# Kernel optimization log

Measured on AMD Instinct MI355X. Metric: run time of the kernel, lower is better.

Reference implementation:

```python
import jax, jax.numpy as jnp
from jax import lax
import numpy as np

B, T, I, H = 256, 512, 512, 1024

def setup_inputs() -> dict:
    key = jax.random.key(0)
    ks = jax.random.split(key, 6)
    s_ih = 1.0 / np.sqrt(H)
    return {
        "x": jax.random.normal(ks[0], (B, T, I), dtype=jnp.float32),
        "W_ih": jax.random.uniform(ks[1], (4 * H, I), minval=-s_ih, maxval=s_ih, dtype=jnp.float32),
        "W_hh": jax.random.uniform(ks[2], (4 * H, H), minval=-s_ih, maxval=s_ih, dtype=jnp.float32),
        "b_ih": jax.random.uniform(ks[3], (4 * H,), minval=-s_ih, maxval=s_ih, dtype=jnp.float32),
        "b_hh": jax.random.uniform(ks[4], (4 * H,), minval=-s_ih, maxval=s_ih, dtype=jnp.float32),
        "c0": jax.random.normal(ks[5], (B, H), dtype=jnp.float32),  # torch code inits cell state with randn
    }

def reference(x, W_ih, W_hh, b_ih, b_hh, c0):
    # Faithful to LSTMBody.forward: h0 = zeros, c0 = randn (provided as input),
    # per-step nn.LSTMCell; returns the final CELL state (the torch code's `out`).
    h0 = jnp.zeros((x.shape[0], W_hh.shape[1]), dtype=x.dtype)
    Wi_T = W_ih.T  # [I, 4H]
    Wh_T = W_hh.T  # [H, 4H]
    b = b_ih + b_hh

    def step(carry, xt):
        h, c = carry
        gates = xt @ Wi_T + h @ Wh_T + b  # [B, 4H]
        i, f, g, o = jnp.split(gates, 4, axis=-1)  # PyTorch gate order: i, f, g, o
        c_new = jax.nn.sigmoid(f) * c + jax.nn.sigmoid(i) * jnp.tanh(g)
        h_new = jax.nn.sigmoid(o) * jnp.tanh(c_new)
        return (h_new, c_new), None

    xs = jnp.swapaxes(x, 0, 1)  # [T, B, I] for scan over time
    (h, c), _ = lax.scan(step, (h0, c0), xs)
    return c
```

## Files before the change

kernel.cpp:

```cpp
#include <hip/hip_runtime.h>
#include <stdint.h>

#define Bsz 256
#define Tsz 512
#define Isz 512
#define Hsz 1024

typedef __attribute__((ext_vector_type(8))) short short8;
typedef __attribute__((ext_vector_type(4))) float f32x4;

static constexpr size_t XBF_OFF  = 0;
static constexpr size_t WIBF_OFF = 134217728;
static constexpr size_t HBUF_OFF = 138412032;
static constexpr size_t FLAG_OFF = 139460608;
static constexpr size_t WS_NEED  = 139493376;

__device__ __forceinline__ unsigned short f2bf(float f) {
  union { float f; unsigned u; } v; v.f = f;
  unsigned r = v.u + 0x7fff + ((v.u >> 16) & 1);
  return (unsigned short)(r >> 16);
}

__device__ __forceinline__ void cvt8(const float* __restrict__ s, unsigned short* __restrict__ d) {
  float4 a = *(const float4*)s;
  float4 b = *(const float4*)(s + 4);
  union { unsigned short us[8]; uint4 v; } o;
  o.us[0] = f2bf(a.x); o.us[1] = f2bf(a.y); o.us[2] = f2bf(a.z); o.us[3] = f2bf(a.w);
  o.us[4] = f2bf(b.x); o.us[5] = f2bf(b.y); o.us[6] = f2bf(b.z); o.us[7] = f2bf(b.w);
  *(uint4*)d = o.v;
}

__device__ __forceinline__ short8 ld_h(const unsigned short* p) {
  unsigned long long lo = __hip_atomic_load((unsigned long long*)(void*)p,
                                            __ATOMIC_RELAXED, __HIP_MEMORY_SCOPE_AGENT);
  unsigned long long hi = __hip_atomic_load((unsigned long long*)(void*)(p + 4),
                                            __ATOMIC_RELAXED, __HIP_MEMORY_SCOPE_AGENT);
  union { unsigned long long q[2]; short8 s; } u;
  u.q[0] = lo; u.q[1] = hi;
  return u.s;
}

__device__ __forceinline__ unsigned ld_flag(const unsigned* p) {
  return __hip_atomic_load((unsigned*)p, __ATOMIC_RELAXED, __HIP_MEMORY_SCOPE_AGENT);
}

__global__ __launch_bounds__(256)
void init_kernel(const float* __restrict__ x, const float* __restrict__ Wi,
                 unsigned char* __restrict__ ws)
{
  unsigned short* xbf  = (unsigned short*)(ws + XBF_OFF);
  unsigned short* wibf = (unsigned short*)(ws + WIBF_OFF);
  const int bid = blockIdx.x;
  const int tid = threadIdx.x;

  if (bid < 32768) {
    const int rowid = bid * 4 + (tid >> 6);
    const int t = rowid >> 8;
    const int b = rowid & 255;
    const int i = (tid & 63) * 8;
    const float* src = x + ((size_t)b * Tsz + t) * Isz + i;
    unsigned short* dst = xbf + (size_t)rowid * Isz + i;
    cvt8(src, dst);
  } else if (bid < 32768 + 1024) {
    const size_t base = (size_t)(bid - 32768) * 2048 + (size_t)tid * 8;
    cvt8(Wi + base, wibf + base);
  } else {
    const int z = bid - 33792;
    uint4 zero = make_uint4(0u, 0u, 0u, 0u);
    for (size_t j = (size_t)z * 256 + tid; j < 67584; j += (size_t)260 * 256)
      ((uint4*)(ws + HBUF_OFF))[j] = zero;
  }
}

__global__ __launch_bounds__(512, 2)
void lstm_persistent(const float* __restrict__ Wh,
                     const float* __restrict__ b_ih, const float* __restrict__ b_hh,
                     const float* __restrict__ c0, float* __restrict__ out,
                     unsigned char* __restrict__ ws)
{
  const unsigned short* __restrict__ xbf  = (const unsigned short*)(ws + XBF_OFF);
  const unsigned short* __restrict__ wibf = (const unsigned short*)(ws + WIBF_OFF);
  unsigned short* __restrict__ hbuf = (unsigned short*)(ws + HBUF_OFF);
  unsigned* __restrict__ flags = (unsigned*)(ws + FLAG_OFF);

  __shared__ unsigned short WhT[64][1032];
  __shared__ float red[4][64][17];
  __shared__ float bias[64];

  const int tid  = threadIdx.x;
  const int bid  = blockIdx.x;
  const int cg   = bid & 63;
  const int rg   = bid >> 6;
  const int wv    = tid >> 6;
  const int wv4   = wv & 3;
  const int khalf = wv >> 2;
  const int lane = tid & 63;
  const int l16  = lane & 15;
  const int quad = lane >> 4;

  {
    const int n  = tid >> 3;
    const int q  = n >> 4, u = n & 15;
    const int gc = q * 1024 + cg * 16 + u;
    const int k0 = (tid & 7) * 128;
    const float* src = Wh + (size_t)gc * Hsz + k0;
    unsigned short* dst = &WhT[n][k0];
    #pragma unroll 4
    for (int k = 0; k < 128; k += 8) cvt8(src + k, dst + k);
  }
  if (tid < 64) {
    const int q = tid >> 4, u = tid & 15;
    const int gc = q * 1024 + cg * 16 + u;
    bias[tid] = b_ih[gc] + b_hh[gc];
  }
  __syncthreads();

  const int rowbase = rg * 64 + wv4 * 16;
  const int arow    = rowbase + l16;
  const int hcol    = cg * 16 + l16;

  unsigned* const flag_base = flags + (size_t)rg * 2048 + (size_t)wv4 * 8;
  unsigned* const myslot    = flag_base + (size_t)cg * 32;
  unsigned* const pollp     = flag_base + (size_t)(khalf * 32 + (lane & 31)) * 32;

  const float bi_r = bias[l16];
  const float bf_r = bias[16 + l16];
  const float bg_r = bias[32 + l16];
  const float bo_r = bias[48 + l16];

  float creg[4] = {0.f, 0.f, 0.f, 0.f};
  if (khalf == 0) {
    #pragma unroll
    for (int r = 0; r < 4; ++r)
      creg[r] = c0[(size_t)(rowbase + quad * 4 + r) * Hsz + hcol];
  }

  const unsigned short* bp[4];
  #pragma unroll
  for (int q = 0; q < 4; ++q)
    bp[q] = wibf + (size_t)(q * 1024 + cg * 16 + l16) * Isz + khalf * 256 + quad * 8;

  int p = 0;
  for (int t = 0; t < Tsz; ++t) {
    const unsigned short* xt = xbf  + (size_t)t * Bsz * Isz + (size_t)arow * Isz
                                    + khalf * 256 + quad * 8;
    const unsigned short* hp = hbuf + (size_t)p * Bsz * Hsz + (size_t)arow * Hsz
                                    + khalf * 512 + quad * 8;
    const unsigned tgt = (unsigned)t;

    f32x4 acc[4];
    #pragma unroll
    for (int q = 0; q < 4; ++q) acc[q] = (f32x4){0.f, 0.f, 0.f, 0.f};

    #pragma unroll
    for (int ks = 0; ks < 8; ++ks) {
      const int kk = ks * 32;
      short8 av = *(const short8*)(xt + kk);
      short8 b0 = *(const short8*)(bp[0] + kk);
      short8 b1 = *(const short8*)(bp[1] + kk);
      short8 b2 = *(const short8*)(bp[2] + kk);
      short8 b3 = *(const short8*)(bp[3] + kk);
      acc[0] = __builtin_amdgcn_mfma_f32_16x16x32_bf16(av, b0, acc[0], 0, 0, 0);
      acc[1] = __builtin_amdgcn_mfma_f32_16x16x32_bf16(av, b1, acc[1], 0, 0, 0);
      acc[2] = __builtin_amdgcn_mfma_f32_16x16x32_bf16(av, b2, acc[2], 0, 0, 0);
      acc[3] = __builtin_amdgcn_mfma_f32_16x16x32_bf16(av, b3, acc[3], 0, 0, 0);
    }

    if (t > 0) {
      unsigned v = ld_flag(pollp);
      while (!__all((int)(v >= tgt))) v = ld_flag(pollp);
      __atomic_signal_fence(__ATOMIC_SEQ_CST);
    }

    short8 hv[8];
    #pragma unroll
    for (int j = 0; j < 8; ++j) hv[j] = ld_h(hp + j * 32);

    const int kbase = khalf * 512;
    #pragma unroll
    for (int ks = 0; ks < 16; ++ks) {
      short8 av = hv[ks & 7];
      if (ks + 8 < 16) hv[ks & 7] = ld_h(hp + (ks + 8) * 32);
      const int kk = kbase + ks * 32;
      short8 b0 = *(const short8*)(&WhT[l16     ][kk + quad * 8]);
      short8 b1 = *(const short8*)(&WhT[16 + l16][kk + quad * 8]);
      short8 b2 = *(const short8*)(&WhT[32 + l16][kk + quad * 8]);
      short8 b3 = *(const short8*)(&WhT[48 + l16][kk + quad * 8]);
      acc[0] = __builtin_amdgcn_mfma_f32_16x16x32_bf16(av, b0, acc[0], 0, 0, 0);
      acc[1] = __builtin_amdgcn_mfma_f32_16x16x32_bf16(av, b1, acc[1], 0, 0, 0);
      acc[2] = __builtin_amdgcn_mfma_f32_16x16x32_bf16(av, b2, acc[2], 0, 0, 0);
      acc[3] = __builtin_amdgcn_mfma_f32_16x16x32_bf16(av, b3, acc[3], 0, 0, 0);
    }

    if (khalf) {
      #pragma unroll
      for (int q = 0; q < 4; ++q)
        #pragma unroll
        for (int r = 0; r < 4; ++r)
          red[wv4][lane][q * 4 + r] = acc[q][r];
    }
    __syncthreads();
    if (!khalf) {
      #pragma unroll
      for (int q = 0; q < 4; ++q)
        #pragma unroll
        for (int r = 0; r < 4; ++r)
          acc[q][r] += red[wv4][lane][q * 4 + r];
    }
    __syncthreads();

    if (!khalf) {
      unsigned short* hn = hbuf + (size_t)(p ^ 1) * Bsz * Hsz;
      #pragma unroll
      for (int r = 0; r < 4; ++r) {
        float gi = acc[0][r] + bi_r;
        float gf = acc[1][r] + bf_r;
        float gg = acc[2][r] + bg_r;
        float go = acc[3][r] + bo_r;
        float si = 1.f / (1.f + __expf(-gi));
        float sf = 1.f / (1.f + __expf(-gf));
        float tg = 1.f - 2.f / (__expf(2.f * gg) + 1.f);
        float so = 1.f / (1.f + __expf(-go));
        float cn = sf * creg[r] + si * tg;
        creg[r] = cn;
        float tc = 1.f - 2.f / (__expf(2.f * cn) + 1.f);
        __hip_atomic_store(&hn[(size_t)(rowbase + quad * 4 + r) * Hsz + hcol],
                           f2bf(so * tc), __ATOMIC_RELAXED, __HIP_MEMORY_SCOPE_AGENT);
      }

      asm volatile("s_waitcnt vmcnt(0)" ::: "memory");
      if (lane == 0)
        __hip_atomic_store(myslot, tgt + 1u, __ATOMIC_RELAXED, __HIP_MEMORY_SCOPE_AGENT);
    }
    p ^= 1;
  }

  if (khalf == 0) {
    #pragma unroll
    for (int r = 0; r < 4; ++r)
      out[(size_t)(rowbase + quad * 4 + r) * Hsz + hcol] = creg[r];
  }
}

extern "C" void kernel_launch(void* const* d_in, const int* in_sizes, int n_in,
                              void* d_out, int out_size, void* d_ws, size_t ws_size,
                              hipStream_t stream) {
  const float* x   = (const float*)d_in[0];
  const float* Wi  = (const float*)d_in[1];
  const float* Wh  = (const float*)d_in[2];
  const float* bih = (const float*)d_in[3];
  const float* bhh = (const float*)d_in[4];
  const float* c0  = (const float*)d_in[5];
  float* out = (float*)d_out;
  unsigned char* ws = (unsigned char*)d_ws;

  if (ws_size < WS_NEED) return;

  init_kernel<<<34052, 256, 0, stream>>>(x, Wi, ws);

  void* args[] = { (void*)&Wh, (void*)&bih, (void*)&bhh,
                   (void*)&c0, (void*)&out, (void*)&ws };
  hipLaunchCooperativeKernel((void*)lstm_persistent, dim3(256), dim3(512),
                             args, 0, stream);
}
```

Baseline: 9.158 ms.

## Aggregate cross-block step flags to one per block with LDS-relayed polling

```diff
diff --git a/kernel.cpp b/kernel.cpp
--- a/kernel.cpp
+++ b/kernel.cpp
@@ -86,6 +86,8 @@
   __shared__ unsigned short WhT[64][1032];
   __shared__ float red[4][64][17];
   __shared__ float bias[64];
+  __shared__ unsigned go01[2];
+  __shared__ unsigned done_cnt;
 
   const int tid  = threadIdx.x;
   const int bid  = blockIdx.x;
@@ -98,6 +100,8 @@
   const int l16  = lane & 15;
   const int quad = lane >> 4;
 
+  if (tid == 0) { go01[0] = 0; go01[1] = 0; done_cnt = 0; }
+
   {
     const int n  = tid >> 3;
     const int q  = n >> 4, u = n & 15;
@@ -119,9 +123,8 @@
   const int arow    = rowbase + l16;
   const int hcol    = cg * 16 + l16;
 
-  unsigned* const flag_base = flags + (size_t)rg * 2048 + (size_t)wv4 * 8;
-  unsigned* const myslot    = flag_base + (size_t)cg * 32;
-  unsigned* const pollp     = flag_base + (size_t)(khalf * 32 + (lane & 31)) * 32;
+  unsigned* const flagrow = flags + (size_t)rg * 64;
+  unsigned* const myflag  = flagrow + cg;
 
   const float bi_r = bias[l16];
   const float bf_r = bias[16 + l16];
@@ -167,8 +170,26 @@
     }
 
     if (t > 0) {
-      unsigned v = ld_flag(pollp);
-      while (!__all((int)(v >= tgt))) v = ld_flag(pollp);
+      if (wv == 7) {
+        unsigned done = 0;
+        do {
+          unsigned v = ld_flag(flagrow + lane);
+          unsigned long long b = __ballot((int)(v >= tgt));
+          if (!(done & 1u) && (unsigned)(b & 0xFFFFFFFFull) == 0xFFFFFFFFu) {
+            if (lane == 0)
+              __hip_atomic_store(&go01[0], tgt, __ATOMIC_RELAXED, __HIP_MEMORY_SCOPE_WORKGROUP);
+            done |= 1u;
+          }
+          if (!(done & 2u) && (unsigned)(b >> 32) == 0xFFFFFFFFu) {
+            if (lane == 0)
+              __hip_atomic_store(&go01[1], tgt, __ATOMIC_RELAXED, __HIP_MEMORY_SCOPE_WORKGROUP);
+            done |= 2u;
+          }
+        } while (done != 3u);
+      } else {
+        while (__hip_atomic_load(&go01[khalf], __ATOMIC_RELAXED, __HIP_MEMORY_SCOPE_WORKGROUP) < tgt)
+          ;
+      }
       __atomic_signal_fence(__ATOMIC_SEQ_CST);
     }
 
@@ -230,7 +251,14 @@
 
       asm volatile("s_waitcnt vmcnt(0)" ::: "memory");
       if (lane == 0)
-        __hip_atomic_store(myslot, tgt + 1u, __ATOMIC_RELAXED, __HIP_MEMORY_SCOPE_AGENT);
+        __hip_atomic_fetch_add(&done_cnt, 1u, __ATOMIC_RELAXED, __HIP_MEMORY_SCOPE_WORKGROUP);
+      if (wv4 == 3 && lane == 0) {
+        while (__hip_atomic_load(&done_cnt, __ATOMIC_RELAXED, __HIP_MEMORY_SCOPE_WORKGROUP)
+               < 4u * (tgt + 1u))
+          ;
+        __atomic_signal_fence(__ATOMIC_SEQ_CST);
+        __hip_atomic_store(myflag, tgt + 1u, __ATOMIC_RELAXED, __HIP_MEMORY_SCOPE_AGENT);
+      }
     }
     p ^= 1;
   }
```

After: 9.026 ms. Within noise of the previous version (-1.4%).
